# Optimization experiments

Measured on AMD Instinct MI355X. Metric: run time of the kernel, lower is better.

## Reference

```python
import jax, jax.numpy as jnp
import numpy as np

B, QLEN, MLEN, E, H, DH = 2, 1024, 1024, 1024, 16, 64
KLEN = QLEN + MLEN
LN_EPS = 1e-3  # keras LayerNormalization default epsilon


def layer_norm(x, gamma, beta):
    mu = jnp.mean(x, axis=-1, keepdims=True)
    var = jnp.mean(jnp.square(x - mu), axis=-1, keepdims=True)
    return (x - mu) * jax.lax.rsqrt(var + LN_EPS) * gamma + beta


def rel_shift(x):
    # x: [B, H, q, k] -> standard Transformer-XL relative shift
    b, h, q, k = x.shape
    x = jnp.pad(x, ((0, 0), (0, 0), (0, 0), (1, 0)))
    x = x.reshape(b, h, k + 1, q)[:, :, 1:, :]
    return x.reshape(b, h, q, k)


def setup_inputs() -> dict:
    key = jax.random.key(0)
    ks = jax.random.split(key, 12)
    s = 0.02
    inp = {
        "w": jax.random.normal(ks[0], (B, QLEN, E), jnp.float32),
        "r": jax.random.normal(ks[1], (1, KLEN, E), jnp.float32),
        "member": jax.random.normal(ks[2], (B, MLEN, E), jnp.float32),
        # causal mask over concatenated keys: 1 = masked
        "attn_mask": (jnp.arange(KLEN)[None, :] > (jnp.arange(QLEN)[:, None] + MLEN)).astype(jnp.float32),
        "Wq": jax.random.normal(ks[3], (E, H * DH), jnp.float32) * s,
        "Wk": jax.random.normal(ks[4], (E, H * DH), jnp.float32) * s,
        "Wv": jax.random.normal(ks[5], (E, H * DH), jnp.float32) * s,
        "Wr": jax.random.normal(ks[6], (E, H * DH), jnp.float32) * s,
        "Wo": jax.random.normal(ks[7], (H * DH, E), jnp.float32) * s,
        "r_w_bias": jnp.zeros((H, DH), jnp.float32),
        "r_r_bias": jnp.zeros((H, DH), jnp.float32),
        "ln1_g": jnp.ones((E,), jnp.float32),
        "ln1_b": jnp.zeros((E,), jnp.float32),
        "W1": jax.random.normal(ks[8], (E, 4 * E), jnp.float32) * s,
        "W2": jax.random.normal(ks[9], (4 * E, E), jnp.float32) * s,
        "ln2_g": jnp.ones((E,), jnp.float32),
        "ln2_b": jnp.zeros((E,), jnp.float32),
    }
    return inp


def reference(w, r, member, attn_mask, Wq, Wk, Wv, Wr, Wo, r_w_bias, r_r_bias,
              ln1_g, ln1_b, W1, W2, ln2_g, ln2_b):
    b, qlen, e = w.shape
    h, dh = r_w_bias.shape
    cat = jnp.concatenate([member, w], axis=1)          # [B, klen, E]
    q = (cat @ Wq)[:, -qlen:]                           # [B, q, H*DH]
    k = cat @ Wk                                        # [B, klen, H*DH]
    v = cat @ Wv
    rp = (r @ Wr)[0]                                    # [klen, H*DH] (shared over batch)
    qh = q.reshape(b, qlen, h, dh)
    kh = k.reshape(b, -1, h, dh)
    vh = v.reshape(b, -1, h, dh)
    rh = rp.reshape(-1, h, dh)
    AC = jnp.einsum('bqhd,bkhd->bhqk', qh + r_w_bias, kh)
    BD = jnp.einsum('bqhd,khd->bhqk', qh + r_r_bias, rh)
    BD = rel_shift(BD)
    attn = (AC + BD) / jnp.sqrt(jnp.float32(e))         # note: scaled by sqrt(embed_size)
    m = attn_mask[None, None]                           # [1,1,q,klen]
    attn = attn * (1.0 - m) - 1e30 * m
    p = jax.nn.softmax(attn, axis=-1)
    o = jnp.einsum('bhqk,bkhd->bqhd', p, vh).reshape(b, qlen, h * dh)
    o = o @ Wo
    x = layer_norm(w + o, ln1_g, ln1_b)
    y = jax.nn.relu(x @ W1) @ W2
    return layer_norm(y + x, ln2_g, ln2_b)
```

## Files before the change

kernel.cpp:

```cpp
#include <hip/hip_runtime.h>
#include <hip/hip_bf16.h>
#include <stdint.h>

typedef __bf16 bf16x8 __attribute__((ext_vector_type(8)));
typedef float  f32x4  __attribute__((ext_vector_type(4)));

constexpr int BB   = 2;
constexpr int QL   = 1024;
constexpr int ML   = 1024;
constexpr int KL   = 2048;
constexpr int ED   = 1024;
constexpr int HH   = 16;
constexpr int FF   = 4096;
constexpr size_t MN = 2048u * 1024u;

__device__ __forceinline__ bf16x8 ld8(const __hip_bfloat16* p) {
    return *reinterpret_cast<const bf16x8*>(p);
}
__device__ __forceinline__ void st8(__hip_bfloat16* p, bf16x8 v) {
    *reinterpret_cast<bf16x8*>(p) = v;
}
__device__ __forceinline__ f32x4 mfma16(bf16x8 a, bf16x8 b, f32x4 c) {
    return __builtin_amdgcn_mfma_f32_16x16x32_bf16(a, b, c, 0, 0, 0);
}
__device__ __forceinline__ void async16(void* lds, const void* g) {
    __builtin_amdgcn_global_load_lds((__attribute__((address_space(1))) void*)g,
                                     (__attribute__((address_space(3))) void*)lds,
                                     16, 0, 0);
}

__global__ __launch_bounds__(256) void build_cat_r(const float* __restrict__ w,
                                                   const float* __restrict__ mem,
                                                   const float* __restrict__ r,
                                                   __hip_bfloat16* __restrict__ cat,
                                                   __hip_bfloat16* __restrict__ rbf) {
    const int bx = blockIdx.x;
    const float* src;
    __hip_bfloat16* dst;
    size_t g;
    if (bx < 2048) {
        size_t t = (size_t)bx * 256 + threadIdx.x;
        g = t * 8;
        int b   = (int)(g >> 21);
        int rem = (int)(g & ((1u << 21) - 1));
        int j = rem >> 10, e = rem & 1023;
        src = (j < ML) ? &mem[((size_t)b * ML + j) * ED + e]
                       : &w[((size_t)b * QL + (j - ML)) * ED + e];
        dst = &cat[g];
    } else {
        g = ((size_t)(bx - 2048) * 256 + threadIdx.x) * 8;
        src = &r[g];
        dst = &rbf[g];
    }
    float4 f0 = *(const float4*)src;
    float4 f1 = *(const float4*)(src + 4);
    union { bf16x8 v; __hip_bfloat16 h[8]; } u;
    u.h[0] = __float2bfloat16(f0.x); u.h[1] = __float2bfloat16(f0.y);
    u.h[2] = __float2bfloat16(f0.z); u.h[3] = __float2bfloat16(f0.w);
    u.h[4] = __float2bfloat16(f1.x); u.h[5] = __float2bfloat16(f1.y);
    u.h[6] = __float2bfloat16(f1.z); u.h[7] = __float2bfloat16(f1.w);
    st8(dst, u.v);
}

__global__ __launch_bounds__(256) void transpose_cast(const float* __restrict__ in,
                                                      __hip_bfloat16* __restrict__ out,
                                                      int K, int N) {
    __shared__ float tile[32][33];
    const int tx = threadIdx.x & 31, ty = threadIdx.x >> 5;
    const int n0 = blockIdx.x * 32, k0 = blockIdx.y * 32;
#pragma unroll
    for (int i = 0; i < 4; ++i)
        tile[ty + i * 8][tx] = in[(size_t)(k0 + ty + i * 8) * N + n0 + tx];
    __syncthreads();
#pragma unroll
    for (int i = 0; i < 4; ++i)
        out[(size_t)(n0 + ty + i * 8) * K + k0 + tx] = __float2bfloat16(tile[tx][ty + i * 8]);
}

__global__ __launch_bounds__(256) void tc5(const float* __restrict__ s0, const float* __restrict__ s1,
                                           const float* __restrict__ s2, const float* __restrict__ s3,
                                           const float* __restrict__ s4,
                                           __hip_bfloat16* __restrict__ wqkvT,
                                           __hip_bfloat16* __restrict__ wot) {
    __shared__ float tile[32][33];
    const int z = blockIdx.z;
    const float* in = (z == 0) ? s0 : (z == 1) ? s1 : (z == 2) ? s2 : (z == 3) ? s3 : s4;
    __hip_bfloat16* out = (z == 4) ? wot : wqkvT + (size_t)z * 1024 * 1024;
    const int tx = threadIdx.x & 31, ty = threadIdx.x >> 5;
    const int n0 = blockIdx.x * 32, k0 = blockIdx.y * 32;
#pragma unroll
    for (int i = 0; i < 4; ++i)
        tile[ty + i * 8][tx] = in[(size_t)(k0 + ty + i * 8) * 1024 + n0 + tx];
    __syncthreads();
#pragma unroll
    for (int i = 0; i < 4; ++i)
        out[(size_t)(n0 + ty + i * 8) * 1024 + k0 + tx] = __float2bfloat16(tile[tx][ty + i * 8]);
}

__global__ __launch_bounds__(256) void transpose_v(const __hip_bfloat16* __restrict__ v,
                                                   __hip_bfloat16* __restrict__ vt) {
    __shared__ __hip_bfloat16 tile[32][33];
    const int tx = threadIdx.x & 31, ty = threadIdx.x >> 5;
    const int s = blockIdx.z, b = s >> 4, h = s & 15;
    const int j0 = blockIdx.x * 32, d0 = blockIdx.y * 32;
#pragma unroll
    for (int i = 0; i < 4; ++i)
        tile[ty + i * 8][tx] =
            v[((size_t)b * KL + j0 + ty + i * 8) * 1024 + h * 64 + d0 + tx];
    __syncthreads();
#pragma unroll
    for (int i = 0; i < 4; ++i)
        vt[((size_t)s * 64 + d0 + ty + i * 8) * KL + j0 + tx] = tile[tx][ty + i * 8];
}

template <int EPI, bool SK>
__global__ __launch_bounds__(256) void gemm_bt(const __hip_bfloat16* __restrict__ A,
                                               const __hip_bfloat16* __restrict__ Bt,
                                               void* __restrict__ Cv,
                                               int N, int kLen, int lda, int ldb) {
    __shared__ __align__(16) __hip_bfloat16 sA[128 * 32];
    __shared__ __align__(16) __hip_bfloat16 sB[128 * 32];
    const int tid = threadIdx.x;
    const int lane = tid & 63;
    const int l16 = lane & 15, quad = lane >> 4;
    const int wv = tid >> 6;
    const int wm = wv >> 1, wn = wv & 1;
    const int bm = blockIdx.y * 128, bn = blockIdx.x * 128;
    const int kOff = SK ? blockIdx.z * kLen : 0;
    const int c0 = tid, c1 = 256 + tid;
    const int r0 = c0 >> 2, o0 = (c0 & 3) * 8;
    const int r1 = c1 >> 2, o1 = (c1 & 3) * 8;
    f32x4 acc[4][4] = {};
    for (int k0 = 0; k0 < kLen; k0 += 32) {
        async16(&sA[c0 * 8], A + (size_t)(bm + r0) * lda + kOff + k0 + o0);
        async16(&sA[c1 * 8], A + (size_t)(bm + r1) * lda + kOff + k0 + o1);
        async16(&sB[c0 * 8], Bt + (size_t)(bn + r0) * ldb + kOff + k0 + o0);
        async16(&sB[c1 * 8], Bt + (size_t)(bn + r1) * ldb + kOff + k0 + o1);
        __syncthreads();
        bf16x8 af[4], bfr[4];
#pragma unroll
        for (int i = 0; i < 4; ++i)
            af[i] = ld8(&sA[(wm * 64 + i * 16 + l16) * 32 + quad * 8]);
#pragma unroll
        for (int j = 0; j < 4; ++j)
            bfr[j] = ld8(&sB[(wn * 64 + j * 16 + l16) * 32 + quad * 8]);
#pragma unroll
        for (int i = 0; i < 4; ++i)
#pragma unroll
            for (int j = 0; j < 4; ++j)
                acc[i][j] = mfma16(af[i], bfr[j], acc[i][j]);
        __syncthreads();
    }
#pragma unroll
    for (int i = 0; i < 4; ++i)
#pragma unroll
        for (int j = 0; j < 4; ++j)
#pragma unroll
            for (int rg = 0; rg < 4; ++rg) {
                size_t row = bm + wm * 64 + i * 16 + quad * 4 + rg;
                size_t col = bn + wn * 64 + j * 16 + l16;
                float v = acc[i][j][rg];
                if (EPI == 0) {
                    float* C = (float*)Cv + (SK ? (size_t)blockIdx.z * MN : 0);
                    C[row * N + col] = v;
                } else {
                    __hip_bfloat16* C = (__hip_bfloat16*)Cv;
                    C[row * N + col] = __float2bfloat16(fmaxf(v, 0.f));
                }
            }
}

__global__ __launch_bounds__(256) void gemm_qkvr(const __hip_bfloat16* __restrict__ cat,
                                                 const __hip_bfloat16* __restrict__ rbf,
                                                 const __hip_bfloat16* __restrict__ Bt,
                                                 __hip_bfloat16* __restrict__ qwb,
                                                 __hip_bfloat16* __restrict__ qrb,
                                                 __hip_bfloat16* __restrict__ kbuf,
                                                 __hip_bfloat16* __restrict__ vbuf,
                                                 __hip_bfloat16* __restrict__ rpb,
                                                 const float* __restrict__ rwb,
                                                 const float* __restrict__ rrb) {
    const int bm = blockIdx.y * 128, bn = blockIdx.x * 128;
    const int region = blockIdx.x >> 3;
    if (region == 0 && (bm & 2047) < 1024) return;
    if (region == 3 && bm >= 2048) return;
    const __hip_bfloat16* A = (region == 3) ? rbf : cat;
    __shared__ __align__(16) __hip_bfloat16 sA[128 * 32];
    __shared__ __align__(16) __hip_bfloat16 sB[128 * 32];
    const int tid = threadIdx.x;
    const int lane = tid & 63;
    const int l16 = lane & 15, quad = lane >> 4;
    const int wv = tid >> 6;
    const int wm = wv >> 1, wn = wv & 1;
    const int c0 = tid, c1 = 256 + tid;
    const int r0 = c0 >> 2, o0 = (c0 & 3) * 8;
    const int r1 = c1 >> 2, o1 = (c1 & 3) * 8;
    f32x4 acc[4][4] = {};
    for (int k0 = 0; k0 < 1024; k0 += 32) {
        async16(&sA[c0 * 8], A + (size_t)(bm + r0) * 1024 + k0 + o0);
        async16(&sA[c1 * 8], A + (size_t)(bm + r1) * 1024 + k0 + o1);
        async16(&sB[c0 * 8], Bt + (size_t)(bn + r0) * 1024 + k0 + o0);
        async16(&sB[c1 * 8], Bt + (size_t)(bn + r1) * 1024 + k0 + o1);
        __syncthreads();
        bf16x8 af[4], bfr[4];
#pragma unroll
        for (int i = 0; i < 4; ++i)
            af[i] = ld8(&sA[(wm * 64 + i * 16 + l16) * 32 + quad * 8]);
#pragma unroll
        for (int j = 0; j < 4; ++j)
            bfr[j] = ld8(&sB[(wn * 64 + j * 16 + l16) * 32 + quad * 8]);
#pragma unroll
        for (int i = 0; i < 4; ++i)
#pragma unroll
            for (int j = 0; j < 4; ++j)
                acc[i][j] = mfma16(af[i], bfr[j], acc[i][j]);
        __syncthreads();
    }
#pragma unroll
    for (int j = 0; j < 4; ++j) {
        const int col = bn + wn * 64 + j * 16 + l16;
        float bw = 0.f, br = 0.f;
        if (region == 0) { bw = rwb[col]; br = rrb[col]; }
#pragma unroll
        for (int i = 0; i < 4; ++i)
#pragma unroll
            for (int rg = 0; rg < 4; ++rg) {
                const int row = bm + wm * 64 + i * 16 + quad * 4 + rg;
                const int bb = row >> 11, jr = row & 2047;
                float v = acc[i][j][rg];
                if (region == 0) {
                    size_t o = ((size_t)(bb * 1024 + (jr - 1024))) * 1024 + col;
                    qwb[o] = __float2bfloat16(v + bw);
                    qrb[o] = __float2bfloat16(v + br);
                } else if (region == 1) {
                    kbuf[((size_t)(bb * 2048 + jr)) * 1024 + (col - 1024)] = __float2bfloat16(v);
                } else if (region == 2) {
                    vbuf[((size_t)(bb * 2048 + jr)) * 1024 + (col - 2048)] = __float2bfloat16(v);
                } else {
                    rpb[(size_t)row * 1024 + (col - 3072)] = __float2bfloat16(v);
                }
            }
    }
}

__global__ __launch_bounds__(128, 2) void flash_attn6(
        const __hip_bfloat16* __restrict__ qw, const __hip_bfloat16* __restrict__ qr,
        const __hip_bfloat16* __restrict__ kbuf, const __hip_bfloat16* __restrict__ vtb,
        const __hip_bfloat16* __restrict__ rpb,
        float* __restrict__ Opart, float* __restrict__ lpart) {
    __shared__ __align__(16) __hip_bfloat16 sk[64][72];
    __shared__ __align__(16) __hip_bfloat16 srp[128][72];
    __shared__ __align__(16) __hip_bfloat16 spb[2][32][72];
    const int tid = threadIdx.x, wv = tid >> 6, lane = tid & 63;
    const int l16 = lane & 15, quad = lane >> 4;
    const int id    = blockIdx.x;
    const int xcd   = id & 7;
    const int rest  = id >> 3;
    const int grp   = rest >> 5;
    const int local = rest & 31;
    const int p     = grp * 8 + xcd;
    const int b = p >> 4, h = p & 15;
    const int qb = local >> 1, chunk = local & 1;
    const int i0b = qb * 64, i0w = i0b + wv * 32;

    bf16x8 qaw[2][2], qar[2][2];
#pragma unroll
    for (int g = 0; g < 2; ++g)
#pragma unroll
        for (int kf = 0; kf < 2; ++kf) {
            size_t qi = ((size_t)(b * QL + i0w + g * 16 + l16)) * 1024 + h * 64 + kf * 32 + quad * 8;
            qaw[g][kf] = ld8(&qw[qi]);
            qar[g][kf] = ld8(&qr[qi]);
        }
    f32x4 oacc[2][4] = {};
    f32x4 lacc[2] = {};
    union { bf16x8 v; __hip_bfloat16 h8[8]; } ou;
#pragma unroll
    for (int j = 0; j < 8; ++j) ou.h8[j] = __float2bfloat16(l16 == 0 ? 1.f : 0.f);
    const bf16x8 onesf = ou.v;

    int srcIdx[4], selr[4];
#pragma unroll
    for (int r = 0; r < 4; ++r) {
        int s = l16 + 15 - (quad * 4 + r);
        selr[r] = s >> 4;
        srcIdx[r] = (lane & 48) | (s & 15);
    }
    const int T = qb + 17, Ta = T >> 1;
    const int t0 = chunk ? Ta : 0, t1 = chunk ? T : Ta;
    const int rbase = 32 - wv * 32;

    for (int jt = t0; jt < t1; ++jt) {
        const int j0 = jt * 64;
        const int ub = j0 - i0b + 960;
#pragma unroll
        for (int pp = 0; pp < 4; ++pp) {
            int cc = pp * 128 + tid, row = cc >> 3, off = (cc & 7) * 8;
            st8(&sk[row][off], ld8(&kbuf[((size_t)(b * KL + j0 + row)) * 1024 + h * 64 + off]));
        }
#pragma unroll
        for (int pp = 0; pp < 8; ++pp) {
            int cc = pp * 128 + tid, row = cc >> 3, off = (cc & 7) * 8;
            int u = ub + row;
            if (u < KL) {
                st8(&srp[row][off], ld8(&rpb[(size_t)u * 1024 + h * 64 + off]));
            } else {
                union { bf16x8 v; uint32_t w[4]; } z;
                z.w[0] = z.w[1] = z.w[2] = z.w[3] = 0u;
                st8(&srp[row][off], z.v);
            }
        }
        bf16x8 vvf[4][2];
#pragma unroll
        for (int dt = 0; dt < 4; ++dt) {
            size_t vr = ((size_t)((b * HH + h) * 64 + dt * 16 + l16)) * 2048 + j0 + quad * 8;
            vvf[dt][0] = ld8(&vtb[vr]);
            vvf[dt][1] = ld8(&vtb[vr + 32]);
        }
        __syncthreads();
        f32x4 sfr[2][4];
#pragma unroll
        for (int nt = 0; nt < 4; ++nt) {
            bf16x8 b0 = ld8(&sk[nt * 16 + l16][quad * 8]);
            bf16x8 b1 = ld8(&sk[nt * 16 + l16][32 + quad * 8]);
#pragma unroll
            for (int g = 0; g < 2; ++g) {
                f32x4 z = {};
                z = mfma16(qaw[g][0], b0, z);
                z = mfma16(qaw[g][1], b1, z);
                sfr[g][nt] = z;
            }
        }
        bf16x8 bF0[6], bF1[6];
#pragma unroll
        for (int t = 0; t < 6; ++t) {
            int rr = rbase + t * 16 + l16;
            bF0[t] = ld8(&srp[rr][quad * 8]);
            bF1[t] = ld8(&srp[rr][32 + quad * 8]);
        }
#pragma unroll
        for (int g = 0; g < 2; ++g) {
            f32x4 bd[5];
#pragma unroll
            for (int t = 0; t < 5; ++t) {
                int ts = t + 1 - g;
                f32x4 z = {};
                z = mfma16(qar[g][0], bF0[ts], z);
                z = mfma16(qar[g][1], bF1[ts], z);
                bd[t] = z;
            }
            float pre[5][4];
#pragma unroll
            for (int t = 0; t < 5; ++t)
#pragma unroll
                for (int r = 0; r < 4; ++r)
                    pre[t][r] = __shfl(bd[t][r], srcIdx[r], 64);
#pragma unroll
            for (int nt = 0; nt < 4; ++nt)
#pragma unroll
                for (int r = 0; r < 4; ++r) {
                    float bdv = selr[r] ? pre[nt + 1][r] : pre[nt][r];
                    float sv = (sfr[g][nt][r] + bdv) * 0.03125f;
                    int ii = i0w + g * 16 + quad * 4 + r;
                    int jj = j0 + nt * 16 + l16;
                    float p_ = (jj <= ii + ML) ? __expf(sv) : 0.f;
                    spb[wv][g * 16 + quad * 4 + r][nt * 16 + l16] = __float2bfloat16(p_);
                }
        }
#pragma unroll
        for (int g = 0; g < 2; ++g) {
            bf16x8 pa0 = ld8(&spb[wv][g * 16 + l16][quad * 8]);
            bf16x8 pa1 = ld8(&spb[wv][g * 16 + l16][32 + quad * 8]);
            lacc[g] = mfma16(pa0, onesf, lacc[g]);
            lacc[g] = mfma16(pa1, onesf, lacc[g]);
#pragma unroll
            for (int dt = 0; dt < 4; ++dt) {
                oacc[g][dt] = mfma16(pa0, vvf[dt][0], oacc[g][dt]);
                oacc[g][dt] = mfma16(pa1, vvf[dt][1], oacc[g][dt]);
            }
        }
        __syncthreads();
    }
    const size_t obase = ((size_t)((chunk * 2 + b) * HH + h)) * (1024 * 64);
#pragma unroll
    for (int g = 0; g < 2; ++g)
#pragma unroll
        for (int dt = 0; dt < 4; ++dt)
#pragma unroll
            for (int r = 0; r < 4; ++r) {
                int q = i0w + g * 16 + quad * 4 + r;
                Opart[obase + (size_t)q * 64 + dt * 16 + l16] = oacc[g][dt][r];
            }
    if (l16 == 0) {
        const size_t lbase = ((size_t)((chunk * 2 + b) * HH + h)) * 1024;
#pragma unroll
        for (int g = 0; g < 2; ++g)
#pragma unroll
            for (int r = 0; r < 4; ++r) {
                int q = i0w + g * 16 + quad * 4 + r;
                lpart[lbase + q] = lacc[g][r];
            }
    }
}

__global__ __launch_bounds__(256) void combine_attn(const float* __restrict__ Opart,
                                                    const float* __restrict__ lpart,
                                                    __hip_bfloat16* __restrict__ og) {
    size_t t = (size_t)blockIdx.x * 256 + threadIdx.x;
    size_t e4 = t * 4;
    int d  = (int)(e4 & 63);
    int q  = (int)((e4 >> 6) & 1023);
    int hh = (int)((e4 >> 16) & 15);
    int bb = (int)(e4 >> 20);
    float ox = 0.f, oy = 0.f, oz = 0.f, ow = 0.f, l = 0.f;
#pragma unroll
    for (int c = 0; c < 2; ++c) {
        size_t gsel = (size_t)((c * 2 + bb) * HH + hh);
        float4 o = *(const float4*)&Opart[gsel * (1024 * 64) + (size_t)q * 64 + d];
        ox += o.x; oy += o.y; oz += o.z; ow += o.w;
        l += lpart[gsel * 1024 + q];
    }
    float inv = 1.f / l;
    union { __hip_bfloat16 h[4]; uint2 u; } o;
    o.h[0] = __float2bfloat16(ox * inv);
    o.h[1] = __float2bfloat16(oy * inv);
    o.h[2] = __float2bfloat16(oz * inv);
    o.h[3] = __float2bfloat16(ow * inv);
    *(uint2*)&og[((size_t)bb * 1024 + q) * 1024 + hh * 64 + d] = o.u;
}

template <int NP, bool WB>
__global__ __launch_bounds__(256) void add_ln_k(const float* __restrict__ res,
                                                const float* __restrict__ parts,
                                                const float* __restrict__ gam,
                                                const float* __restrict__ bet,
                                                float* __restrict__ of,
                                                __hip_bfloat16* __restrict__ ob) {
    const int tid = threadIdx.x;
    const size_t base = (size_t)blockIdx.x * ED;
    const int col = tid * 4;
    float4 va = *(const float4*)&res[base + col];
    float x0 = va.x, x1 = va.y, x2 = va.z, x3 = va.w;
#pragma unroll
    for (int z = 0; z < NP; ++z) {
        float4 p = *(const float4*)&parts[(size_t)z * MN + base + col];
        x0 += p.x; x1 += p.y; x2 += p.z; x3 += p.w;
    }
    float s1 = x0 + x1 + x2 + x3;
    float s2 = x0 * x0 + x1 * x1 + x2 * x2 + x3 * x3;
    for (int o = 32; o > 0; o >>= 1) {
        s1 += __shfl_down(s1, o, 64);
        s2 += __shfl_down(s2, o, 64);
    }
    __shared__ float p1[4], p2[4];
    if ((tid & 63) == 0) { p1[tid >> 6] = s1; p2[tid >> 6] = s2; }
    __syncthreads();
    float S1 = p1[0] + p1[1] + p1[2] + p1[3];
    float S2 = p2[0] + p2[1] + p2[2] + p2[3];
    float mu = S1 * (1.0f / ED);
    float var = S2 * (1.0f / ED) - mu * mu;
    float rs = rsqrtf(var + 1e-3f);
    float4 g4 = *(const float4*)&gam[col];
    float4 b4 = *(const float4*)&bet[col];
    float y0 = (x0 - mu) * rs * g4.x + b4.x;
    float y1 = (x1 - mu) * rs * g4.y + b4.y;
    float y2 = (x2 - mu) * rs * g4.z + b4.z;
    float y3 = (x3 - mu) * rs * g4.w + b4.w;
    *(float4*)&of[base + col] = make_float4(y0, y1, y2, y3);
    if (WB) {
        ob[base + col + 0] = __float2bfloat16(y0);
        ob[base + col + 1] = __float2bfloat16(y1);
        ob[base + col + 2] = __float2bfloat16(y2);
        ob[base + col + 3] = __float2bfloat16(y3);
    }
}

extern "C" void kernel_launch(void* const* d_in, const int* in_sizes, int n_in,
                              void* d_out, int out_size, void* d_ws, size_t ws_size,
                              hipStream_t stream) {
    const float* w   = (const float*)d_in[0];
    const float* r   = (const float*)d_in[1];
    const float* mem = (const float*)d_in[2];
    const float* Wq  = (const float*)d_in[4];
    const float* Wk  = (const float*)d_in[5];
    const float* Wv  = (const float*)d_in[6];
    const float* Wr  = (const float*)d_in[7];
    const float* Wo  = (const float*)d_in[8];
    const float* rwb = (const float*)d_in[9];
    const float* rrb = (const float*)d_in[10];
    const float* g1  = (const float*)d_in[11];
    const float* b1  = (const float*)d_in[12];
    const float* W1  = (const float*)d_in[13];
    const float* W2  = (const float*)d_in[14];
    const float* g2  = (const float*)d_in[15];
    const float* b2  = (const float*)d_in[16];

    char* ws = (char*)d_ws;
    size_t off = 0;
    auto alloc = [&](size_t bytes) -> void* {
        void* p = ws + off;
        off += (bytes + 255) & ~(size_t)255;
        return p;
    };
    __hip_bfloat16* wqkvT = (__hip_bfloat16*)alloc((size_t)4096 * 1024 * 2);
    __hip_bfloat16* wot   = (__hip_bfloat16*)alloc((size_t)ED * ED * 2);
    __hip_bfloat16* w1t   = (__hip_bfloat16*)alloc((size_t)FF * ED * 2);
    __hip_bfloat16* w2t   = (__hip_bfloat16*)alloc((size_t)ED * FF * 2);
    __hip_bfloat16* qwb   = (__hip_bfloat16*)alloc((size_t)BB * QL * ED * 2);
    __hip_bfloat16* qrb   = (__hip_bfloat16*)alloc((size_t)BB * QL * ED * 2);
    __hip_bfloat16* vtb   = (__hip_bfloat16*)alloc((size_t)BB * KL * ED * 2);
    __hip_bfloat16* rpb   = (__hip_bfloat16*)alloc((size_t)KL * ED * 2);
    __hip_bfloat16* og    = (__hip_bfloat16*)alloc((size_t)BB * QL * ED * 2);
    char* regA = (char*)alloc((size_t)BB * KL * ED * 2);
    __hip_bfloat16* cat = (__hip_bfloat16*)regA;
    float*          xf  = (float*)regA;
    char* regB = (char*)alloc((size_t)KL * ED * 2);
    __hip_bfloat16* rbf = (__hip_bfloat16*)regB;
    __hip_bfloat16* xb  = (__hip_bfloat16*)regB;
    char* regC = (char*)alloc((size_t)BB * QL * FF * 2);
    __hip_bfloat16* kbuf = (__hip_bfloat16*)regC;
    __hip_bfloat16* vbuf = (__hip_bfloat16*)(regC + (size_t)BB * KL * ED * 2);
    __hip_bfloat16* y1   = (__hip_bfloat16*)regC;
    const size_t opartBytes = (size_t)4 * HH * QL * 64 * 4;
    const size_t lpartBytes = (size_t)4 * HH * QL * 4;
    size_t regEsz = opartBytes + lpartBytes;
    if (regEsz < (size_t)4 * MN * 4) regEsz = (size_t)4 * MN * 4;
    char* regE = (char*)alloc(regEsz);
    float* Opart  = (float*)regE;
    float* lpart  = (float*)(regE + opartBytes);
    float* o_part = (float*)regE;
    float* f_part = (float*)regE;
    if (off > ws_size) return;

    build_cat_r<<<3072, 256, 0, stream>>>(w, mem, r, cat, rbf);
    tc5<<<dim3(32, 32, 5), 256, 0, stream>>>(Wq, Wk, Wv, Wr, Wo, wqkvT, wot);
    transpose_cast<<<dim3(128, 32), 256, 0, stream>>>(W1, w1t, 1024, 4096);
    transpose_cast<<<dim3(32, 128), 256, 0, stream>>>(W2, w2t, 4096, 1024);

    gemm_qkvr<<<dim3(32, 32), 256, 0, stream>>>(cat, rbf, wqkvT, qwb, qrb, kbuf, vbuf, rpb,
                                                rwb, rrb);
    transpose_v<<<dim3(64, 2, 32), 256, 0, stream>>>(vbuf, vtb);

    flash_attn6<<<dim3(1024), 128, 0, stream>>>(qwb, qrb, kbuf, vtb, rpb, Opart, lpart);
    combine_attn<<<2048, 256, 0, stream>>>(Opart, lpart, og);

    gemm_bt<0, true><<<dim3(8, 16, 4), 256, 0, stream>>>(og, wot, o_part, 1024, 256, 1024, 1024);
    add_ln_k<4, true><<<2048, 256, 0, stream>>>(w, o_part, g1, b1, xf, xb);

    gemm_bt<2, false><<<dim3(32, 16, 1), 256, 0, stream>>>(xb, w1t, y1, 4096, 1024, 1024, 1024);
    gemm_bt<0, true><<<dim3(8, 16, 4), 256, 0, stream>>>(y1, w2t, f_part, 1024, 1024, 4096, 4096);
    add_ln_k<4, false><<<2048, 256, 0, stream>>>(xf, f_part, g2, b2, (float*)d_out, nullptr);
}
```

Measured before the change: 461.0 us.

## Load rel-pos fragments directly from global in attention and compact QKVR grid

The attention kernel stops staging the relative-position rows in shared memory. Each wave now loads its own B-operand fragments straight from global memory, clamping out-of-range rows instead of zero-filling them. This removes a large LDS buffer and its store/load traffic, at the cost of redundant global reads across waves. The XCD-aware block remapping is replaced by a plain 3D grid, and the QKVR GEMM launches only the tiles that do useful work instead of early-exiting empty ones.

```diff
diff --git a/kernel.cpp b/kernel.cpp
--- a/kernel.cpp
+++ b/kernel.cpp
@@ -180,10 +180,29 @@
                                                  __hip_bfloat16* __restrict__ rpb,
                                                  const float* __restrict__ rwb,
                                                  const float* __restrict__ rrb) {
-    const int bm = blockIdx.y * 128, bn = blockIdx.x * 128;
-    const int region = blockIdx.x >> 3;
-    if (region == 0 && (bm & 2047) < 1024) return;
-    if (region == 3 && bm >= 2048) return;
+    const int id = blockIdx.x;
+    int region, bm, bn;
+    if (id < 128) {
+        region = 0;
+        int i = id, bmI = i >> 3;
+        bm = (bmI >> 3) * 2048 + 1024 + (bmI & 7) * 128;
+        bn = (i & 7) * 128;
+    } else if (id < 384) {
+        region = 1;
+        int i = id - 128;
+        bm = (i >> 3) * 128;
+        bn = (8 + (i & 7)) * 128;
+    } else if (id < 640) {
+        region = 2;
+        int i = id - 384;
+        bm = (i >> 3) * 128;
+        bn = (16 + (i & 7)) * 128;
+    } else {
+        region = 3;
+        int i = id - 640;
+        bm = (i >> 3) * 128;
+        bn = (24 + (i & 7)) * 128;
+    }
     const __hip_bfloat16* A = (region == 3) ? rbf : cat;
     __shared__ __align__(16) __hip_bfloat16 sA[128 * 32];
     __shared__ __align__(16) __hip_bfloat16 sB[128 * 32];
@@ -243,24 +262,17 @@
     }
 }
 
-__global__ __launch_bounds__(128, 2) void flash_attn6(
+__global__ __launch_bounds__(128, 2) void flash_attn7(
         const __hip_bfloat16* __restrict__ qw, const __hip_bfloat16* __restrict__ qr,
         const __hip_bfloat16* __restrict__ kbuf, const __hip_bfloat16* __restrict__ vtb,
         const __hip_bfloat16* __restrict__ rpb,
         float* __restrict__ Opart, float* __restrict__ lpart) {
     __shared__ __align__(16) __hip_bfloat16 sk[64][72];
-    __shared__ __align__(16) __hip_bfloat16 srp[128][72];
     __shared__ __align__(16) __hip_bfloat16 spb[2][32][72];
     const int tid = threadIdx.x, wv = tid >> 6, lane = tid & 63;
     const int l16 = lane & 15, quad = lane >> 4;
-    const int id    = blockIdx.x;
-    const int xcd   = id & 7;
-    const int rest  = id >> 3;
-    const int grp   = rest >> 5;
-    const int local = rest & 31;
-    const int p     = grp * 8 + xcd;
-    const int b = p >> 4, h = p & 15;
-    const int qb = local >> 1, chunk = local & 1;
+    const int qb = blockIdx.x >> 1, chunk = blockIdx.x & 1;
+    const int h = blockIdx.y, b = blockIdx.z;
     const int i0b = qb * 64, i0w = i0b + wv * 32;
 
     bf16x8 qaw[2][2], qar[2][2];
@@ -288,27 +300,14 @@
     }
     const int T = qb + 17, Ta = T >> 1;
     const int t0 = chunk ? Ta : 0, t1 = chunk ? T : Ta;
-    const int rbase = 32 - wv * 32;
+    const __hip_bfloat16* rB = rpb + h * 64;
 
     for (int jt = t0; jt < t1; ++jt) {
         const int j0 = jt * 64;
-        const int ub = j0 - i0b + 960;
 #pragma unroll
         for (int pp = 0; pp < 4; ++pp) {
             int cc = pp * 128 + tid, row = cc >> 3, off = (cc & 7) * 8;
             st8(&sk[row][off], ld8(&kbuf[((size_t)(b * KL + j0 + row)) * 1024 + h * 64 + off]));
-        }
-#pragma unroll
-        for (int pp = 0; pp < 8; ++pp) {
-            int cc = pp * 128 + tid, row = cc >> 3, off = (cc & 7) * 8;
-            int u = ub + row;
-            if (u < KL) {
-                st8(&srp[row][off], ld8(&rpb[(size_t)u * 1024 + h * 64 + off]));
-            } else {
-                union { bf16x8 v; uint32_t w[4]; } z;
-                z.w[0] = z.w[1] = z.w[2] = z.w[3] = 0u;
-                st8(&srp[row][off], z.v);
-            }
         }
         bf16x8 vvf[4][2];
 #pragma unroll
@@ -316,6 +315,16 @@
             size_t vr = ((size_t)((b * HH + h) * 64 + dt * 16 + l16)) * 2048 + j0 + quad * 8;
             vvf[dt][0] = ld8(&vtb[vr]);
             vvf[dt][1] = ld8(&vtb[vr + 32]);
+        }
+        bf16x8 bF0[6], bF1[6];
+        const int ubase = j0 - i0w + 992;
+#pragma unroll
+        for (int t = 0; t < 6; ++t) {
+            int u = ubase + t * 16 + l16;
+            if (u > 2047) u = 2047;
+            const __hip_bfloat16* rr = rB + (size_t)u * 1024 + quad * 8;
+            bF0[t] = ld8(rr);
+            bF1[t] = ld8(rr + 32);
         }
         __syncthreads();
         f32x4 sfr[2][4];
@@ -330,13 +339,6 @@
                 z = mfma16(qaw[g][1], b1, z);
                 sfr[g][nt] = z;
             }
-        }
-        bf16x8 bF0[6], bF1[6];
-#pragma unroll
-        for (int t = 0; t < 6; ++t) {
-            int rr = rbase + t * 16 + l16;
-            bF0[t] = ld8(&srp[rr][quad * 8]);
-            bF1[t] = ld8(&srp[rr][32 + quad * 8]);
         }
 #pragma unroll
         for (int g = 0; g < 2; ++g) {
@@ -537,11 +539,11 @@
     transpose_cast<<<dim3(128, 32), 256, 0, stream>>>(W1, w1t, 1024, 4096);
     transpose_cast<<<dim3(32, 128), 256, 0, stream>>>(W2, w2t, 4096, 1024);
 
-    gemm_qkvr<<<dim3(32, 32), 256, 0, stream>>>(cat, rbf, wqkvT, qwb, qrb, kbuf, vbuf, rpb,
-                                                rwb, rrb);
+    gemm_qkvr<<<dim3(768), 256, 0, stream>>>(cat, rbf, wqkvT, qwb, qrb, kbuf, vbuf, rpb,
+                                             rwb, rrb);
     transpose_v<<<dim3(64, 2, 32), 256, 0, stream>>>(vbuf, vtb);
 
-    flash_attn6<<<dim3(1024), 128, 0, stream>>>(qwb, qrb, kbuf, vtb, rpb, Opart, lpart);
+    flash_attn7<<<dim3(32, 16, 2), 128, 0, stream>>>(qwb, qrb, kbuf, vtb, rpb, Opart, lpart);
     combine_attn<<<2048, 256, 0, stream>>>(Opart, lpart, og);
 
     gemm_bt<0, true><<<dim3(8, 16, 4), 256, 0, stream>>>(og, wot, o_part, 1024, 256, 1024, 1024);
```

After: 394.0 us. 1.17x faster.
